# Performance work log

Measured on AMD Instinct MI355X. Metric: run time of the kernel, lower is better.

## Reference

```python
import jax, jax.numpy as jnp
import numpy as np

SHAPES = [(4, 48, 48), (2, 24, 24), (1, 12, 12), (1, 6, 6)]  # (D,H,W) per level
B, E, NH, NL, NP, DF, NLAYERS = 2, 256, 8, 4, 4, 1024, 6
HD = E // NH
LEVEL_SIZES = [d * h * w for d, h, w in SHAPES]
LEVEL_START = [0] + [int(s) for s in np.cumsum(LEVEL_SIZES)[:-1]]
S = int(sum(LEVEL_SIZES))
PARAM_KEYS = ['W_off', 'b_off', 'W_attn', 'b_attn', 'W_val', 'b_val', 'W_out', 'b_out',
              'ln1_g', 'ln1_b', 'W_ff1', 'b_ff1', 'W_ff2', 'b_ff2', 'ln2_g', 'ln2_b']


def setup_inputs() -> dict:
    key = jax.random.key(0)
    ks = jax.random.split(key, 32)
    inp = {}
    for i, (d, h, w) in enumerate(SHAPES):
        inp[f'feat{i}'] = jax.random.normal(ks[i], (B, E, d, h, w), jnp.float32)
        inp[f'pos{i}'] = jax.random.normal(ks[4 + i], (B, E, d, h, w), jnp.float32)
    inp['level_embed'] = jax.random.normal(ks[8], (NL, E), jnp.float32)
    nrm = lambda k, shape, s: jax.random.normal(k, shape, jnp.float32) * s
    inp['W_off'] = nrm(ks[9], (NLAYERS, E, NH * NL * NP * 3), 0.01)
    inp['b_off'] = nrm(ks[10], (NLAYERS, NH * NL * NP * 3), 1.0)
    inp['W_attn'] = nrm(ks[11], (NLAYERS, E, NH * NL * NP), 0.02)
    inp['b_attn'] = jnp.zeros((NLAYERS, NH * NL * NP), jnp.float32)
    inp['W_val'] = nrm(ks[12], (NLAYERS, E, E), E ** -0.5)
    inp['b_val'] = jnp.zeros((NLAYERS, E), jnp.float32)
    inp['W_out'] = nrm(ks[13], (NLAYERS, E, E), E ** -0.5)
    inp['b_out'] = jnp.zeros((NLAYERS, E), jnp.float32)
    inp['ln1_g'] = jnp.ones((NLAYERS, E), jnp.float32)
    inp['ln1_b'] = jnp.zeros((NLAYERS, E), jnp.float32)
    inp['W_ff1'] = nrm(ks[14], (NLAYERS, E, DF), E ** -0.5)
    inp['b_ff1'] = jnp.zeros((NLAYERS, DF), jnp.float32)
    inp['W_ff2'] = nrm(ks[15], (NLAYERS, DF, E), DF ** -0.5)
    inp['b_ff2'] = jnp.zeros((NLAYERS, E), jnp.float32)
    inp['ln2_g'] = jnp.ones((NLAYERS, E), jnp.float32)
    inp['ln2_b'] = jnp.zeros((NLAYERS, E), jnp.float32)
    return inp


def _layer_norm(x, g, b):
    m = jnp.mean(x, -1, keepdims=True)
    v = jnp.mean((x - m) ** 2, -1, keepdims=True)
    return (x - m) * jax.lax.rsqrt(v + 1e-5) * g + b


def _ref_points():
    # all-zero padding masks -> valid_ratios == 1, so reference points are the
    # normalized voxel centers, identical across levels. Returns (S, 3) in (x, y, z).
    refs = []
    for (D, H, W) in SHAPES:
        z = (jnp.arange(D, dtype=jnp.float32) + 0.5) / D
        y = (jnp.arange(H, dtype=jnp.float32) + 0.5) / H
        x = (jnp.arange(W, dtype=jnp.float32) + 0.5) / W
        zz, yy, xx = jnp.meshgrid(z, y, x, indexing='ij')
        refs.append(jnp.stack([xx.ravel(), yy.ravel(), zz.ravel()], -1))
    return jnp.concatenate(refs, 0)


def _sample_level(v, coords, w, D, H, W):
    # v: (B, NH, N_lvl, HD) flattened level values
    # coords: (B, NH, S, NP, 3) pixel-space coords (x, y, z), align_corners=False convention
    # w: (B, NH, S, NP) attention weights (folded into trilinear corner weights)
    cx, cy, cz = coords[..., 0], coords[..., 1], coords[..., 2]
    x0, y0, z0 = jnp.floor(cx), jnp.floor(cy), jnp.floor(cz)
    fx, fy, fz = cx - x0, cy - y0, cz - z0
    Bq, Hq, Sq, Pq = w.shape
    acc = jnp.zeros((Bq, Hq, Sq, HD), v.dtype)
    for dz in (0, 1):
        wz = fz if dz else 1.0 - fz
        iz = z0 + dz
        for dy in (0, 1):
            wy = fy if dy else 1.0 - fy
            iy = y0 + dy
            for dx in (0, 1):
                wx = fx if dx else 1.0 - fx
                ix = x0 + dx
                valid = (ix >= 0) & (ix < W) & (iy >= 0) & (iy < H) & (iz >= 0) & (iz < D)
                wgt = w * wx * wy * wz * valid  # zero-padding outside the volume
                idx = ((jnp.clip(iz, 0, D - 1) * H + jnp.clip(iy, 0, H - 1)) * W
                       + jnp.clip(ix, 0, W - 1)).astype(jnp.int32)
                g = jnp.take_along_axis(v, idx.reshape(Bq, Hq, Sq * Pq)[..., None], axis=2)
                g = g.reshape(Bq, Hq, Sq, Pq, HD)
                acc = acc + jnp.einsum('bhsp,bhspd->bhsd', wgt, g)
    return acc


def _deform_attn(x, pos, ref, normalizer, p, sample_fn):
    B_, S_, _ = x.shape
    q = x + pos
    value = (x @ p['W_val'] + p['b_val']).reshape(B_, S_, NH, HD).transpose(0, 2, 1, 3)
    off = (q @ p['W_off'] + p['b_off']).reshape(B_, S_, NH, NL, NP, 3)
    attn = jax.nn.softmax((q @ p['W_attn'] + p['b_attn']).reshape(B_, S_, NH, NL * NP), -1)
    attn = attn.reshape(B_, S_, NH, NL, NP)
    # normalized sampling locations in [0,1]^3 (x, y, z)
    loc = ref[None, :, None, None, None, :] + off / normalizer[None, None, None, :, None, :]
    out = jnp.zeros((B_, NH, S_, HD), x.dtype)
    for lvl, (D, H, W) in enumerate(SHAPES):
        s0, n = LEVEL_START[lvl], LEVEL_SIZES[lvl]
        v = value[:, :, s0:s0 + n]
        size = jnp.array([W, H, D], x.dtype)
        coords = (loc[:, :, :, lvl] * size - 0.5).transpose(0, 2, 1, 3, 4)  # (B,NH,S,NP,3)
        w = attn[:, :, :, lvl].transpose(0, 2, 1, 3)  # (B,NH,S,NP)
        out = out + sample_fn(v, coords, w, D, H, W)
    out = out.transpose(0, 2, 1, 3).reshape(B_, S_, E)
    return out @ p['W_out'] + p['b_out']


def _encoder_layer(x, pos, ref, normalizer, p, sample_fn):
    x = _layer_norm(x + _deform_attn(x, pos, ref, normalizer, p, sample_fn),
                    p['ln1_g'], p['ln1_b'])
    h = jax.nn.relu(x @ p['W_ff1'] + p['b_ff1']) @ p['W_ff2'] + p['b_ff2']
    return _layer_norm(x + h, p['ln2_g'], p['ln2_b'])


def _forward(feats, poss, level_embed, params, sample_fn):
    x = jnp.concatenate([f.reshape(f.shape[0], E, -1).transpose(0, 2, 1) for f in feats], axis=1)
    pos = jnp.concatenate(
        [poss[l].reshape(poss[l].shape[0], E, -1).transpose(0, 2, 1) + level_embed[l]
         for l in range(NL)], axis=1)
    ref = _ref_points()
    normalizer = jnp.array([[w, h, d] for d, h, w in SHAPES], jnp.float32)  # (NL,3) (x,y,z)
    for l in range(NLAYERS):
        p = {k: params[k][l] for k in PARAM_KEYS}
        x = _encoder_layer(x, pos, ref, normalizer, p, sample_fn)
    return x


def reference(feat0, feat1, feat2, feat3, pos0, pos1, pos2, pos3, level_embed,
              W_off, b_off, W_attn, b_attn, W_val, b_val, W_out, b_out,
              ln1_g, ln1_b, W_ff1, b_ff1, W_ff2, b_ff2, ln2_g, ln2_b):
    params = dict(W_off=W_off, b_off=b_off, W_attn=W_attn, b_attn=b_attn,
                  W_val=W_val, b_val=b_val, W_out=W_out, b_out=b_out,
                  ln1_g=ln1_g, ln1_b=ln1_b, W_ff1=W_ff1, b_ff1=b_ff1,
                  W_ff2=W_ff2, b_ff2=b_ff2, ln2_g=ln2_g, ln2_b=ln2_b)
    return _forward([feat0, feat1, feat2, feat3], [pos0, pos1, pos2, pos3],
                    level_embed, params, _sample_level)
```

## Files before the change

### kernel.cpp

```cpp
#include <hip/hip_runtime.h>

#define S_TOT   10548
#define M_ROWS  21096
#define M_PAD   21120
#define E_DIM   256
#define NH_DIM  8
#define HD_DIM  32
#define DF_DIM  1024
#define NLAYERS 6

typedef unsigned short ushort_t;
typedef __attribute__((ext_vector_type(8))) short bf16x8;
typedef __attribute__((ext_vector_type(4))) float f32x4;

__device__ inline ushort_t f2bf(float f) {
    unsigned u = __float_as_uint(f);
    u += 0x7FFF + ((u >> 16) & 1);
    return (ushort_t)(u >> 16);
}
__device__ inline float bf2f(ushort_t h) {
    return __uint_as_float(((unsigned)h) << 16);
}
__device__ inline f32x4 up2(unsigned a, unsigned b) {
    f32x4 v;
// ... 129 lines not shown
        __syncthreads();
        if (k0 + 32 < K) {
            const int nxt = cur ^ 1;
            gload16(Ag + k0 + 32, (ushort_t*)&As[nxt][(w * 16) * 32]);
            #pragma unroll
            for (int q = 0; q < 4; ++q)
                gload16(Bg + (size_t)(q * 16) * K + k0 + 32,
                        (ushort_t*)&Bs[nxt][(w * 64 + q * 16) * 32]);
        }
        bf16x8 af[4], bfr[4];
        #pragma unroll
        for (int i = 0; i < 4; ++i)
            af[i] = *(const bf16x8*)&As[cur][(i * 16 + lrow) * 32 + rs];
        #pragma unroll
        for (int j = 0; j < 4; ++j)
            bfr[j] = *(const bf16x8*)&Bs[cur][(wn + j * 16 + lrow) * 32 + rs];
        #pragma unroll
        for (int i = 0; i < 4; ++i)
            #pragma unroll
            for (int j = 0; j < 4; ++j)
                acc[i][j] = __builtin_amdgcn_mfma_f32_16x16x32_bf16(af[i], bfr[j], acc[i][j], 0, 0, 0);
    }

    #pragma unroll
    for (int j = 0; j < 4; ++j) {
        int col = wn + j * 16 + lrow;
        float bia = (sup == 0) ? b1[col]
                  : (sup == 1) ? b2[col]
                  : (col < 128) ? b2[256 + col] : b3[col - 128];
        #pragma unroll
        for (int i = 0; i < 4; ++i)
            #pragma unroll
            for (int rg = 0; rg < 4; ++rg) {
                int row = row0 + i * 16 + quad * 4 + rg;
                if (row < M) {
                    float v = acc[i][j][rg] + bia;
                    if (sup == 0) {
                        int b = (row >= S_TOT) ? 1 : 0;
                        int s = row - b * S_TOT;
                        O1[(((size_t)(b * NH_DIM + (col >> 5))) * S_TOT + s) * HD_DIM + (col & 31)] = f2bf(v);
                    } else if (sup == 2 && col >= 128) {
                        int acol = col - 128;
                        O3[((size_t)(acol >> 4) * M_ROWS + row) * 16 + (acol & 15)] = f2bf(v);
                    } else {
                        int ocol = (sup == 1) ? col : 256 + col;
                        int hh = (ocol * 1366) >> 16;
                        O2[((size_t)hh * M_ROWS + row) * 48 + (ocol - hh * 48)] = f2bf(v);
                    }
                }
            }
    }
}

__global__ __launch_bounds__(256, 4)
void gemm_ln(const ushort_t* __restrict__ A, const ushort_t* __restrict__ Bt,
             const float* __restrict__ bias,
             float* __restrict__ x, ushort_t* __restrict__ xb,
             const float* __restrict__ lng, const float* __restrict__ lnb,
             int M)
{
    __shared__ short As[2][32 * 32];
    __shared__ short Bs[2][256 * 32];
    float* red1 = (float*)&As[0][0];
    float* red2 = red1 + 32 * 5;
    const int K = 256;
    int t    = threadIdx.x;
    int row0 = blockIdx.x * 32;
    int lane = t & 63;
    int w    = t >> 6;
    int wn   = w * 64;
    const int quad = lane >> 4, lrow = lane & 15;

    f32x4 acc[2][4];
    #pragma unroll
    for (int i = 0; i < 2; ++i)
        #pragma unroll
        for (int j = 0; j < 4; ++j)
            acc[i][j] = (f32x4){0.f, 0.f, 0.f, 0.f};

    int srow = lane >> 2;
    const int sw = (((lane & 3) ^ ((lane >> 3) & 3)) * 8);
    const int rs = ((quad ^ ((lrow >> 1) & 3)) * 8);
    const ushort_t* Ag = A + (size_t)(row0 + w * 16 + srow) * K + sw;
    const ushort_t* Bg = Bt + (size_t)(w * 64 + srow) * K + sw;

    if (w < 2) gload16(Ag, (ushort_t*)&As[0][(w * 16) * 32]);
    #pragma unroll
    for (int q = 0; q < 4; ++q)
        gload16(Bg + (size_t)(q * 16) * K,
                (ushort_t*)&Bs[0][(w * 64 + q * 16) * 32]);

    #pragma unroll
    for (int k0 = 0; k0 < K; k0 += 32) {
        const int cur = (k0 >> 5) & 1;
        __syncthreads();
        if (k0 + 32 < K) {
            const int nxt = cur ^ 1;
            if (w < 2) gload16(Ag + k0 + 32, (ushort_t*)&As[nxt][(w * 16) * 32]);
            #pragma unroll
            for (int q = 0; q < 4; ++q)
                gload16(Bg + (size_t)(q * 16) * K + k0 + 32,
                        (ushort_t*)&Bs[nxt][(w * 64 + q * 16) * 32]);
        }
        bf16x8 af[2], bfr[4];
        #pragma unroll
        for (int i = 0; i < 2; ++i)
            af[i] = *(const bf16x8*)&As[cur][(i * 16 + lrow) * 32 + rs];
        #pragma unroll
        for (int j = 0; j < 4; ++j)
            bfr[j] = *(const bf16x8*)&Bs[cur][(wn + j * 16 + lrow) * 32 + rs];
        #pragma unroll
        for (int i = 0; i < 2; ++i)
            #pragma unroll
            for (int j = 0; j < 4; ++j)
                acc[i][j] = __builtin_amdgcn_mfma_f32_16x16x32_bf16(af[i], bfr[j], acc[i][j], 0, 0, 0);
    }

    float gj[4], bj[4], bi[4];
    #pragma unroll
    for (int j = 0; j < 4; ++j) {
        int col = wn + j * 16 + lrow;
        gj[j] = lng[col];
        bj[j] = lnb[col];
        bi[j] = bias[col];
    }

    #pragma unroll
    for (int i = 0; i < 2; ++i)
        #pragma unroll
        for (int rg = 0; rg < 4; ++rg) {
            int row = row0 + i * 16 + quad * 4 + rg;
            #pragma unroll
            for (int j = 0; j < 4; ++j) {
                int col = wn + j * 16 + lrow;
                float xres = (row < M) ? x[(size_t)row * 256 + col] : 0.f;
                acc[i][j][rg] += bi[j] + xres;
            }
            float p1 = acc[i][0][rg] + acc[i][1][rg] + acc[i][2][rg] + acc[i][3][rg];
            float p2 = acc[i][0][rg] * acc[i][0][rg] + acc[i][1][rg] * acc[i][1][rg]
                     + acc[i][2][rg] * acc[i][2][rg] + acc[i][3][rg] * acc[i][3][rg];
            p1 += __shfl_xor(p1, 1); p2 += __shfl_xor(p2, 1);
            p1 += __shfl_xor(p1, 2); p2 += __shfl_xor(p2, 2);
            p1 += __shfl_xor(p1, 4); p2 += __shfl_xor(p2, 4);
            p1 += __shfl_xor(p1, 8); p2 += __shfl_xor(p2, 8);
            if (lrow == 0) {
                int rl = i * 16 + quad * 4 + rg;
                red1[rl * 5 + w] = p1;
                red2[rl * 5 + w] = p2;
            }
        }
    __syncthreads();

    #pragma unroll
    for (int i = 0; i < 2; ++i)
        #pragma unroll
        for (int rg = 0; rg < 4; ++rg) {
            int rl = i * 16 + quad * 4 + rg;
            float S1 = red1[rl * 5 + 0] + red1[rl * 5 + 1] + red1[rl * 5 + 2] + red1[rl * 5 + 3];
            float S2 = red2[rl * 5 + 0] + red2[rl * 5 + 1] + red2[rl * 5 + 2] + red2[rl * 5 + 3];
            float mean = S1 * (1.f / 256);
            float rstd = rsqrtf(S2 * (1.f / 256) - mean * mean + 1e-5f);
            int row = row0 + rl;
            if (row < M) {
                #pragma unroll
                for (int j = 0; j < 4; ++j) {
                    int col = wn + j * 16 + lrow;
                    float out = (acc[i][j][rg] - mean) * rstd * gj[j] + bj[j];
                    size_t o = (size_t)row * 256 + col;
                    x[o]  = out;
                    xb[o] = f2bf(out);
                }
            }
        }
}

__global__ __launch_bounds__(256, 2)
void ffn_kernel(const ushort_t* __restrict__ Axb, const ushort_t* __restrict__ W1t,
                const ushort_t* __restrict__ W2t,
                const float* __restrict__ bias1, const float* __restrict__ bias2,
                float* __restrict__ x, ushort_t* __restrict__ xb,
                ushort_t* __restrict__ qb, const ushort_t* __restrict__ posb,
                const float* __restrict__ lng, const float* __restrict__ lnb,
                int M)
{
    __shared__ short As[2][32 * 32];
    __shared__ short Bs[2][256 * 32];
    __shared__ short Hs[32 * 264];
    float* red1 = (float*)&As[0][0];
    float* red2 = red1 + 32 * 5;
    const int K = 256;
    int t    = threadIdx.x;
    int row0 = blockIdx.x * 32;
    int lane = t & 63;
    int w    = t >> 6;
    int wn   = w * 64;
    const int quad = lane >> 4, lrow = lane & 15;
    int srow = lane >> 2;
    const int sw = (((lane & 3) ^ ((lane >> 3) & 3)) * 8);
    const int rs = ((quad ^ ((lrow >> 1) & 3)) * 8);

    f32x4 acc[2][4];
    #pragma unroll
    for (int i = 0; i < 2; ++i)
        #pragma unroll
        for (int j = 0; j < 4; ++j)
            acc[i][j] = (f32x4){0.f, 0.f, 0.f, 0.f};

    const ushort_t* Ag = Axb + (size_t)(row0 + w * 16 + srow) * K + sw;

    for (int c = 0; c < 4; ++c) {
        f32x4 hh[2][4];
        #pragma unroll
        for (int i = 0; i < 2; ++i)
            #pragma unroll
            for (int j = 0; j < 4; ++j)
                hh[i][j] = (f32x4){0.f, 0.f, 0.f, 0.f};

        const ushort_t* B1g = W1t + (size_t)(c * 256 + w * 64 + srow) * K + sw;

        __syncthreads();
        if (w < 2) gload16(Ag, (ushort_t*)&As[0][(w * 16) * 32]);
        #pragma unroll
        for (int q = 0; q < 4; ++q)
            gload16(B1g + (size_t)(q * 16) * K,
                    (ushort_t*)&Bs[0][(w * 64 + q * 16) * 32]);

        #pragma unroll
        for (int k0 = 0; k0 < K; k0 += 32) {
            const int cur = (k0 >> 5) & 1;
            __syncthreads();
            if (k0 + 32 < K) {
                const int nxt = cur ^ 1;
                if (w < 2) gload16(Ag + k0 + 32, (ushort_t*)&As[nxt][(w * 16) * 32]);
                #pragma unroll
                for (int q = 0; q < 4; ++q)
                    gload16(B1g + (size_t)(q * 16) * K + k0 + 32,
                            (ushort_t*)&Bs[nxt][(w * 64 + q * 16) * 32]);
            }
            bf16x8 af[2], bfr[4];
            #pragma unroll
            for (int i = 0; i < 2; ++i)
                af[i] = *(const bf16x8*)&As[cur][(i * 16 + lrow) * 32 + rs];
            #pragma unroll
            for (int j = 0; j < 4; ++j)
                bfr[j] = *(const bf16x8*)&Bs[cur][(wn + j * 16 + lrow) * 32 + rs];
            #pragma unroll
            for (int i = 0; i < 2; ++i)
                #pragma unroll
                for (int j = 0; j < 4; ++j)
                    hh[i][j] = __builtin_amdgcn_mfma_f32_16x16x32_bf16(af[i], bfr[j], hh[i][j], 0, 0, 0);
        }

        #pragma unroll
        for (int j = 0; j < 4; ++j) {
            int col = wn + j * 16 + lrow;
            float b1v = bias1[c * 256 + col];
            #pragma unroll
            for (int i = 0; i < 2; ++i)
                #pragma unroll
                for (int rg = 0; rg < 4; ++rg) {
                    int rl = i * 16 + quad * 4 + rg;
                    Hs[rl * 264 + col] = f2bf(fmaxf(hh[i][j][rg] + b1v, 0.f));
                }
        }
        __syncthreads();

        const ushort_t* B2g = W2t + (size_t)(w * 64 + srow) * 1024 + c * 256 + sw;
        #pragma unroll
        for (int q = 0; q < 4; ++q)
            gload16(B2g + (size_t)(q * 16) * 1024,
                    (ushort_t*)&Bs[0][(w * 64 + q * 16) * 32]);

        #pragma unroll
        for (int k0 = 0; k0 < 256; k0 += 32) {
            const int cur = (k0 >> 5) & 1;
            __syncthreads();
            if (k0 + 32 < 256) {
                const int nxt = cur ^ 1;
                #pragma unroll
                for (int q = 0; q < 4; ++q)
                    gload16(B2g + (size_t)(q * 16) * 1024 + k0 + 32,
                            (ushort_t*)&Bs[nxt][(w * 64 + q * 16) * 32]);
            }
            bf16x8 af[2], bfr[4];
            #pragma unroll
            for (int i = 0; i < 2; ++i)
                af[i] = *(const bf16x8*)&Hs[(i * 16 + lrow) * 264 + k0 + quad * 8];
            #pragma unroll
            for (int j = 0; j < 4; ++j)
                bfr[j] = *(const bf16x8*)&Bs[cur][(wn + j * 16 + lrow) * 32 + rs];
            #pragma unroll
            for (int i = 0; i < 2; ++i)
                #pragma unroll
                for (int j = 0; j < 4; ++j)
                    acc[i][j] = __builtin_amdgcn_mfma_f32_16x16x32_bf16(af[i], bfr[j], acc[i][j], 0, 0, 0);
        }
    }

    float gj[4], bj[4], bi[4];
    #pragma unroll
    for (int j = 0; j < 4; ++j) {
        int col = wn + j * 16 + lrow;
        gj[j] = lng[col];
        bj[j] = lnb[col];
        bi[j] = bias2[col];
    }

    #pragma unroll
    for (int i = 0; i < 2; ++i)
        #pragma unroll
        for (int rg = 0; rg < 4; ++rg) {
            int row = row0 + i * 16 + quad * 4 + rg;
            #pragma unroll
            for (int j = 0; j < 4; ++j) {
                int col = wn + j * 16 + lrow;
                float xres = (row < M) ? x[(size_t)row * 256 + col] : 0.f;
                acc[i][j][rg] += bi[j] + xres;
            }
            float p1 = acc[i][0][rg] + acc[i][1][rg] + acc[i][2][rg] + acc[i][3][rg];
            float p2 = acc[i][0][rg] * acc[i][0][rg] + acc[i][1][rg] * acc[i][1][rg]
                     + acc[i][2][rg] * acc[i][2][rg] + acc[i][3][rg] * acc[i][3][rg];
            p1 += __shfl_xor(p1, 1); p2 += __shfl_xor(p2, 1);
            p1 += __shfl_xor(p1, 2); p2 += __shfl_xor(p2, 2);
            p1 += __shfl_xor(p1, 4); p2 += __shfl_xor(p2, 4);
            p1 += __shfl_xor(p1, 8); p2 += __shfl_xor(p2, 8);
            if (lrow == 0) {
                int rl = i * 16 + quad * 4 + rg;
                red1[rl * 5 + w] = p1;
                red2[rl * 5 + w] = p2;
            }
        }
    __syncthreads();

    #pragma unroll
    for (int i = 0; i < 2; ++i)
        #pragma unroll
        for (int rg = 0; rg < 4; ++rg) {
            int rl = i * 16 + quad * 4 + rg;
            float S1 = red1[rl * 5 + 0] + red1[rl * 5 + 1] + red1[rl * 5 + 2] + red1[rl * 5 + 3];
            float S2 = red2[rl * 5 + 0] + red2[rl * 5 + 1] + red2[rl * 5 + 2] + red2[rl * 5 + 3];
            float mean = S1 * (1.f / 256);
            float rstd = rsqrtf(S2 * (1.f / 256) - mean * mean + 1e-5f);
            int row = row0 + rl;
            if (row < M) {
                #pragma unroll
                for (int j = 0; j < 4; ++j) {
                    int col = wn + j * 16 + lrow;
                    float out = (acc[i][j][rg] - mean) * rstd * gj[j] + bj[j];
                    size_t o = (size_t)row * 256 + col;
                    x[o]  = out;
                    xb[o] = f2bf(out);
                    qb[o] = f2bf(out + bf2f(posb[o]));
                }
            }
        }
}

__global__ __launch_bounds__(256, 4)
void sample_kernel(const ushort_t* __restrict__ valueb,
                   const ushort_t* __restrict__ offh,
                   const ushort_t* __restrict__ attnh,
                   ushort_t* __restrict__ sampb)
{
    __shared__ float wrec[16 * 168];
    __shared__ int   idxA[16 * 40];

    const int LD_[4]  = {4, 2, 1, 1};
    const int LH_[4]  = {48, 24, 12, 6};
    const int LW_[4]  = {48, 24, 12, 6};
    const int LS0_[4] = {0, 9216, 10368, 10512};

    int t   = threadIdx.x;
    int gl  = t >> 4;
    int sub = t & 15;
    int h   = blockIdx.x;
    int r   = blockIdx.y * 16 + gl;
    bool valid = (r < M_ROWS);
    if (!valid) r = M_ROWS - 1;
    int b   = (r >= S_TOT) ? 1 : 0;
    int s   = r - b * S_TOT;

    float rx, ry, rz;
    {
        int j;
        if (s < 9216)       { j = s;         int qx = j % 48; int q2 = j / 48; int qy = q2 % 48; int qz = q2 / 48;
                              rx = (qx + 0.5f) * (1.f/48); ry = (qy + 0.5f) * (1.f/48); rz = (qz + 0.5f) * (1.f/4); }
        else if (s < 10368) { j = s - 9216;  int qx = j % 24; int q2 = j / 24; int qy = q2 % 24; int qz = q2 / 24;
                              rx = (qx + 0.5f) * (1.f/24); ry = (qy + 0.5f) * (1.f/24); rz = (qz + 0.5f) * (1.f/2); }
        else if (s < 10512) { j = s - 10368; int qx = j % 12; int qy = j / 12;
                              rx = (qx + 0.5f) * (1.f/12); ry = (qy + 0.5f) * (1.f/12); rz = 0.5f; }
        else                { j = s - 10512; int qx = j % 6;  int qy = j / 6;
                              rx = (qx + 0.5f) * (1.f/6);  ry = (qy + 0.5f) * (1.f/6);  rz = 0.5f; }
    }

    {
        int p = sub;
        float lg = bf2f(attnh[((size_t)h * M_ROWS + r) * 16 + p]);
        float mx = lg;
        mx = fmaxf(mx, __shfl_xor(mx, 1));
        mx = fmaxf(mx, __shfl_xor(mx, 2));
        mx = fmaxf(mx, __shfl_xor(mx, 4));
        mx = fmaxf(mx, __shfl_xor(mx, 8));
        float e = __expf(lg - mx);
        float sm = e;
        sm += __shfl_xor(sm, 1);
        sm += __shfl_xor(sm, 2);
        sm += __shfl_xor(sm, 4);
        sm += __shfl_xor(sm, 8);
// ... 60 lines not shown
    accA.z += __shfl_xor(accA.z, 8); accA.w += __shfl_xor(accA.w, 8);
    accB.x += __shfl_xor(accB.x, 8); accB.y += __shfl_xor(accB.y, 8);
    accB.z += __shfl_xor(accB.z, 8); accB.w += __shfl_xor(accB.w, 8);

    if (cr == 0 && valid) {
        ushort4 o1, o2;
        o1.x = f2bf(accA.x); o1.y = f2bf(accA.y); o1.z = f2bf(accA.z); o1.w = f2bf(accA.w);
        o2.x = f2bf(accB.x); o2.y = f2bf(accB.y); o2.z = f2bf(accB.z); o2.w = f2bf(accB.w);
        ushort_t* op = sampb + (size_t)r * E_DIM + h * HD_DIM + q * 8;
        *(ushort4*)op       = o1;
        *(ushort4*)(op + 4) = o2;
    }
}

extern "C" void kernel_launch(void* const* d_in, const int* in_sizes, int n_in,
                              void* d_out, int out_size, void* d_ws, size_t ws_size,
                              hipStream_t stream)
{
    const float* f0     = (const float*)d_in[0];
    const float* p0     = (const float*)d_in[1];
    const float* f1     = (const float*)d_in[2];
    const float* p1     = (const float*)d_in[3];
    const float* f2     = (const float*)d_in[4];
    const float* p2     = (const float*)d_in[5];
    const float* f3     = (const float*)d_in[6];
    const float* p3     = (const float*)d_in[7];
    const float* lemb   = (const float*)d_in[8];
    const float* W_off  = (const float*)d_in[9];
    const float* b_off  = (const float*)d_in[10];
    const float* W_attn = (const float*)d_in[11];
    const float* b_attn = (const float*)d_in[12];
    const float* W_val  = (const float*)d_in[13];
    const float* b_val  = (const float*)d_in[14];
    const float* W_out  = (const float*)d_in[15];
    const float* b_out  = (const float*)d_in[16];
    const float* ln1_g  = (const float*)d_in[17];
    const float* ln1_b  = (const float*)d_in[18];
    const float* W_ff1  = (const float*)d_in[19];
    const float* b_ff1  = (const float*)d_in[20];
    const float* W_ff2  = (const float*)d_in[21];
    const float* b_ff2  = (const float*)d_in[22];
    const float* ln2_g  = (const float*)d_in[23];
    const float* ln2_b  = (const float*)d_in[24];

    float* x = (float*)d_out;
    char*  w = (char*)d_ws;

    ushort_t* posb   = (ushort_t*)(w + 0);
    ushort_t* valueb = (ushort_t*)(w + 21626880 + 262144);
    char*     region =            (w + 34525184);
    ushort_t* offh   = (ushort_t*)(region);
    ushort_t* attnh  = (ushort_t*)(region + 16220160);
    ushort_t* sampb  = (ushort_t*)(region + 21626880);
    ushort_t* xb     = (ushort_t*)(w + 77778944);
    ushort_t* qb     = (ushort_t*)(w + 88592384);
    ushort_t* wb     = (ushort_t*)(w + 99405824);

    ushort_t* Wc_t = wb;
    ushort_t* Wp_t = wb + 1179648;
    ushort_t* W1_t = wb + 1572864;
    ushort_t* W2_t = wb + 3145728;

    dim3 blk(256);

    transpose_cvt_kernel<<<dim3(8, 8, 6),  blk, 0, stream>>>(W_val,  Wc_t, 256, 256,  196608, 0);
    transpose_cvt_kernel<<<dim3(12, 8, 6), blk, 0, stream>>>(W_off,  Wc_t, 256, 384,  196608, 256);
    transpose_cvt_kernel<<<dim3(4, 8, 6),  blk, 0, stream>>>(W_attn, Wc_t, 256, 128,  196608, 640);
    transpose_cvt_kernel<<<dim3(8, 8, 6),  blk, 0, stream>>>(W_out,  Wp_t, 256, 256,   65536, 0);
    transpose_cvt_kernel<<<dim3(32, 8, 6), blk, 0, stream>>>(W_ff1,  W1_t, 256, 1024, 262144, 0);
    transpose_cvt_kernel<<<dim3(8, 32, 6), blk, 0, stream>>>(W_ff2,  W2_t, 1024, 256, 262144, 0);

    assemble_kernel<<<dim3(331, 8, 2), blk, 0, stream>>>(
        f0, p0, f1, p1, f2, p2, f3, p3, lemb, x, posb, xb, qb);

    const int MT = M_PAD / 64;
    const int LT = M_PAD / 32;
    const int SB = (M_ROWS + 15) / 16;
    for (int l = 0; l < NLAYERS; ++l) {
        gemm_part1<<<dim3(3, MT), blk, 0, stream>>>(
            xb, qb, Wc_t + l * 196608,
            b_val + l * 256, b_off + l * 384, b_attn + l * 128,
            valueb, offh, attnh, M_ROWS);
        sample_kernel<<<dim3(NH_DIM, SB), blk, 0, stream>>>(valueb, offh, attnh, sampb);
        gemm_ln<<<LT, blk, 0, stream>>>(
            sampb, Wp_t + l * 65536, b_out + l * 256,
            x, xb, ln1_g + l * 256, ln1_b + l * 256, M_ROWS);
        ffn_kernel<<<LT, blk, 0, stream>>>(
            xb, W1_t + l * 262144, W2_t + l * 262144,
            b_ff1 + l * 1024, b_ff2 + l * 256,
            x, xb, qb, posb,
            ln2_g + l * 256, ln2_b + l * 256, M_ROWS);
    }
}
```

Before: 1.116 ms.

## Fuse output projection and LayerNorm1 into the FFN kernel

Merges the output-projection GEMM with its residual add and first LayerNorm into the FFN kernel. The normalized rows stay in a shared-memory tile (Xs) that feeds the FFN's first GEMM, and the fp32 residual stays in registers for the second LayerNorm. This removes one kernel launch per layer and the global write and re-read of x/xb between the two stages. In exchange the fused kernel needs more registers and shared memory, which may reduce occupancy.

```diff
diff --git a/kernel.cpp b/kernel.cpp
--- a/kernel.cpp
+++ b/kernel.cpp
@@ -205,140 +205,21 @@
     }
 }
 
-__global__ __launch_bounds__(256, 4)
-void gemm_ln(const ushort_t* __restrict__ A, const ushort_t* __restrict__ Bt,
-             const float* __restrict__ bias,
-             float* __restrict__ x, ushort_t* __restrict__ xb,
-             const float* __restrict__ lng, const float* __restrict__ lnb,
-             int M)
-{
-    __shared__ short As[2][32 * 32];
-    __shared__ short Bs[2][256 * 32];
-    float* red1 = (float*)&As[0][0];
-    float* red2 = red1 + 32 * 5;
-    const int K = 256;
-    int t    = threadIdx.x;
-    int row0 = blockIdx.x * 32;
-    int lane = t & 63;
-    int w    = t >> 6;
-    int wn   = w * 64;
-    const int quad = lane >> 4, lrow = lane & 15;
-
-    f32x4 acc[2][4];
-    #pragma unroll
-    for (int i = 0; i < 2; ++i)
-        #pragma unroll
-        for (int j = 0; j < 4; ++j)
-            acc[i][j] = (f32x4){0.f, 0.f, 0.f, 0.f};
-
-    int srow = lane >> 2;
-    const int sw = (((lane & 3) ^ ((lane >> 3) & 3)) * 8);
-    const int rs = ((quad ^ ((lrow >> 1) & 3)) * 8);
-    const ushort_t* Ag = A + (size_t)(row0 + w * 16 + srow) * K + sw;
-    const ushort_t* Bg = Bt + (size_t)(w * 64 + srow) * K + sw;
-
-    if (w < 2) gload16(Ag, (ushort_t*)&As[0][(w * 16) * 32]);
-    #pragma unroll
-    for (int q = 0; q < 4; ++q)
-        gload16(Bg + (size_t)(q * 16) * K,
-                (ushort_t*)&Bs[0][(w * 64 + q * 16) * 32]);
-
-    #pragma unroll
-    for (int k0 = 0; k0 < K; k0 += 32) {
-        const int cur = (k0 >> 5) & 1;
-        __syncthreads();
-        if (k0 + 32 < K) {
-            const int nxt = cur ^ 1;
-            if (w < 2) gload16(Ag + k0 + 32, (ushort_t*)&As[nxt][(w * 16) * 32]);
-            #pragma unroll
-            for (int q = 0; q < 4; ++q)
-                gload16(Bg + (size_t)(q * 16) * K + k0 + 32,
-                        (ushort_t*)&Bs[nxt][(w * 64 + q * 16) * 32]);
-        }
-        bf16x8 af[2], bfr[4];
-        #pragma unroll
-        for (int i = 0; i < 2; ++i)
-            af[i] = *(const bf16x8*)&As[cur][(i * 16 + lrow) * 32 + rs];
-        #pragma unroll
-        for (int j = 0; j < 4; ++j)
-            bfr[j] = *(const bf16x8*)&Bs[cur][(wn + j * 16 + lrow) * 32 + rs];
-        #pragma unroll
-        for (int i = 0; i < 2; ++i)
-            #pragma unroll
-            for (int j = 0; j < 4; ++j)
-                acc[i][j] = __builtin_amdgcn_mfma_f32_16x16x32_bf16(af[i], bfr[j], acc[i][j], 0, 0, 0);
-    }
-
-    float gj[4], bj[4], bi[4];
-    #pragma unroll
-    for (int j = 0; j < 4; ++j) {
-        int col = wn + j * 16 + lrow;
-        gj[j] = lng[col];
-        bj[j] = lnb[col];
-        bi[j] = bias[col];
-    }
-
-    #pragma unroll
-    for (int i = 0; i < 2; ++i)
-        #pragma unroll
-        for (int rg = 0; rg < 4; ++rg) {
-            int row = row0 + i * 16 + quad * 4 + rg;
-            #pragma unroll
-            for (int j = 0; j < 4; ++j) {
-                int col = wn + j * 16 + lrow;
-                float xres = (row < M) ? x[(size_t)row * 256 + col] : 0.f;
-                acc[i][j][rg] += bi[j] + xres;
-            }
-            float p1 = acc[i][0][rg] + acc[i][1][rg] + acc[i][2][rg] + acc[i][3][rg];
-            float p2 = acc[i][0][rg] * acc[i][0][rg] + acc[i][1][rg] * acc[i][1][rg]
-                     + acc[i][2][rg] * acc[i][2][rg] + acc[i][3][rg] * acc[i][3][rg];
-            p1 += __shfl_xor(p1, 1); p2 += __shfl_xor(p2, 1);
-            p1 += __shfl_xor(p1, 2); p2 += __shfl_xor(p2, 2);
-            p1 += __shfl_xor(p1, 4); p2 += __shfl_xor(p2, 4);
-            p1 += __shfl_xor(p1, 8); p2 += __shfl_xor(p2, 8);
-            if (lrow == 0) {
-                int rl = i * 16 + quad * 4 + rg;
-                red1[rl * 5 + w] = p1;
-                red2[rl * 5 + w] = p2;
-            }
-        }
-    __syncthreads();
-
-    #pragma unroll
-    for (int i = 0; i < 2; ++i)
-        #pragma unroll
-        for (int rg = 0; rg < 4; ++rg) {
-            int rl = i * 16 + quad * 4 + rg;
-            float S1 = red1[rl * 5 + 0] + red1[rl * 5 + 1] + red1[rl * 5 + 2] + red1[rl * 5 + 3];
-            float S2 = red2[rl * 5 + 0] + red2[rl * 5 + 1] + red2[rl * 5 + 2] + red2[rl * 5 + 3];
-            float mean = S1 * (1.f / 256);
-            float rstd = rsqrtf(S2 * (1.f / 256) - mean * mean + 1e-5f);
-            int row = row0 + rl;
-            if (row < M) {
-                #pragma unroll
-                for (int j = 0; j < 4; ++j) {
-                    int col = wn + j * 16 + lrow;
-                    float out = (acc[i][j][rg] - mean) * rstd * gj[j] + bj[j];
-                    size_t o = (size_t)row * 256 + col;
-                    x[o]  = out;
-                    xb[o] = f2bf(out);
-                }
-            }
-        }
-}
-
 __global__ __launch_bounds__(256, 2)
-void ffn_kernel(const ushort_t* __restrict__ Axb, const ushort_t* __restrict__ W1t,
-                const ushort_t* __restrict__ W2t,
-                const float* __restrict__ bias1, const float* __restrict__ bias2,
-                float* __restrict__ x, ushort_t* __restrict__ xb,
-                ushort_t* __restrict__ qb, const ushort_t* __restrict__ posb,
-                const float* __restrict__ lng, const float* __restrict__ lnb,
-                int M)
+void ln_ffn_kernel(const ushort_t* __restrict__ Asamp, const ushort_t* __restrict__ Wpt,
+                   const float* __restrict__ biasP,
+                   const float* __restrict__ ln1g, const float* __restrict__ ln1b,
+                   const ushort_t* __restrict__ W1t, const ushort_t* __restrict__ W2t,
+                   const float* __restrict__ bias1, const float* __restrict__ bias2,
+                   float* __restrict__ x, ushort_t* __restrict__ xb,
+                   ushort_t* __restrict__ qb, const ushort_t* __restrict__ posb,
+                   const float* __restrict__ ln2g, const float* __restrict__ ln2b,
+                   int M)
 {
     __shared__ short As[2][32 * 32];
     __shared__ short Bs[2][256 * 32];
     __shared__ short Hs[32 * 264];
+    __shared__ short Xs[32 * 264];
     float* red1 = (float*)&As[0][0];
     float* red2 = red1 + 32 * 5;
     const int K = 256;
@@ -352,30 +233,21 @@
     const int sw = (((lane & 3) ^ ((lane >> 3) & 3)) * 8);
     const int rs = ((quad ^ ((lrow >> 1) & 3)) * 8);
 
-    f32x4 acc[2][4];
+    f32x4 accL[2][4];
     #pragma unroll
     for (int i = 0; i < 2; ++i)
         #pragma unroll
         for (int j = 0; j < 4; ++j)
-            acc[i][j] = (f32x4){0.f, 0.f, 0.f, 0.f};
-
-    const ushort_t* Ag = Axb + (size_t)(row0 + w * 16 + srow) * K + sw;
-
-    for (int c = 0; c < 4; ++c) {
-        f32x4 hh[2][4];
-        #pragma unroll
-        for (int i = 0; i < 2; ++i)
-            #pragma unroll
-            for (int j = 0; j < 4; ++j)
-                hh[i][j] = (f32x4){0.f, 0.f, 0.f, 0.f};
-
-        const ushort_t* B1g = W1t + (size_t)(c * 256 + w * 64 + srow) * K + sw;
-
-        __syncthreads();
+            accL[i][j] = (f32x4){0.f, 0.f, 0.f, 0.f};
+
+    {
+        const ushort_t* Ag = Asamp + (size_t)(row0 + w * 16 + srow) * K + sw;
+        const ushort_t* Bg = Wpt + (size_t)(w * 64 + srow) * K + sw;
+
         if (w < 2) gload16(Ag, (ushort_t*)&As[0][(w * 16) * 32]);
         #pragma unroll
         for (int q = 0; q < 4; ++q)
-            gload16(B1g + (size_t)(q * 16) * K,
+            gload16(Bg + (size_t)(q * 16) * K,
                     (ushort_t*)&Bs[0][(w * 64 + q * 16) * 32]);
 
         #pragma unroll
@@ -387,13 +259,118 @@
                 if (w < 2) gload16(Ag + k0 + 32, (ushort_t*)&As[nxt][(w * 16) * 32]);
                 #pragma unroll
                 for (int q = 0; q < 4; ++q)
+                    gload16(Bg + (size_t)(q * 16) * K + k0 + 32,
+                            (ushort_t*)&Bs[nxt][(w * 64 + q * 16) * 32]);
+            }
+            bf16x8 af[2], bfr[4];
+            #pragma unroll
+            for (int i = 0; i < 2; ++i)
+                af[i] = *(const bf16x8*)&As[cur][(i * 16 + lrow) * 32 + rs];
+            #pragma unroll
+            for (int j = 0; j < 4; ++j)
+                bfr[j] = *(const bf16x8*)&Bs[cur][(wn + j * 16 + lrow) * 32 + rs];
+            #pragma unroll
+            for (int i = 0; i < 2; ++i)
+                #pragma unroll
+                for (int j = 0; j < 4; ++j)
+                    accL[i][j] = __builtin_amdgcn_mfma_f32_16x16x32_bf16(af[i], bfr[j], accL[i][j], 0, 0, 0);
+        }
+    }
+
+    f32x4 resid[2][4];
+    {
+        float gj[4], bj[4], bi[4];
+        #pragma unroll
+        for (int j = 0; j < 4; ++j) {
+            int col = wn + j * 16 + lrow;
+            gj[j] = ln1g[col];
+            bj[j] = ln1b[col];
+            bi[j] = biasP[col];
+        }
+
+        #pragma unroll
+        for (int i = 0; i < 2; ++i)
+            #pragma unroll
+            for (int rg = 0; rg < 4; ++rg) {
+                int row = row0 + i * 16 + quad * 4 + rg;
+                #pragma unroll
+                for (int j = 0; j < 4; ++j) {
+                    int col = wn + j * 16 + lrow;
+                    float xres = (row < M) ? x[(size_t)row * 256 + col] : 0.f;
+                    accL[i][j][rg] += bi[j] + xres;
+                }
+                float p1 = accL[i][0][rg] + accL[i][1][rg] + accL[i][2][rg] + accL[i][3][rg];
+                float p2 = accL[i][0][rg] * accL[i][0][rg] + accL[i][1][rg] * accL[i][1][rg]
+                         + accL[i][2][rg] * accL[i][2][rg] + accL[i][3][rg] * accL[i][3][rg];
+                p1 += __shfl_xor(p1, 1); p2 += __shfl_xor(p2, 1);
+                p1 += __shfl_xor(p1, 2); p2 += __shfl_xor(p2, 2);
+                p1 += __shfl_xor(p1, 4); p2 += __shfl_xor(p2, 4);
+                p1 += __shfl_xor(p1, 8); p2 += __shfl_xor(p2, 8);
+                if (lrow == 0) {
+                    int rl = i * 16 + quad * 4 + rg;
+                    red1[rl * 5 + w] = p1;
+                    red2[rl * 5 + w] = p2;
+                }
+            }
+        __syncthreads();
+
+        #pragma unroll
+        for (int i = 0; i < 2; ++i)
+            #pragma unroll
+            for (int rg = 0; rg < 4; ++rg) {
+                int rl = i * 16 + quad * 4 + rg;
+                float S1 = red1[rl * 5 + 0] + red1[rl * 5 + 1] + red1[rl * 5 + 2] + red1[rl * 5 + 3];
+                float S2 = red2[rl * 5 + 0] + red2[rl * 5 + 1] + red2[rl * 5 + 2] + red2[rl * 5 + 3];
+                float mean = S1 * (1.f / 256);
+                float rstd = rsqrtf(S2 * (1.f / 256) - mean * mean + 1e-5f);
+                #pragma unroll
+                for (int j = 0; j < 4; ++j) {
+                    int col = wn + j * 16 + lrow;
+                    float out = (accL[i][j][rg] - mean) * rstd * gj[j] + bj[j];
+                    resid[i][j][rg] = out;
+                    Xs[rl * 264 + col] = f2bf(out);
+                }
+            }
+    }
+
+    f32x4 acc[2][4];
+    #pragma unroll
+    for (int i = 0; i < 2; ++i)
+        #pragma unroll
+        for (int j = 0; j < 4; ++j)
+            acc[i][j] = (f32x4){0.f, 0.f, 0.f, 0.f};
+
+    for (int c = 0; c < 4; ++c) {
+        f32x4 hh[2][4];
+        #pragma unroll
+        for (int i = 0; i < 2; ++i)
+            #pragma unroll
+            for (int j = 0; j < 4; ++j)
+                hh[i][j] = (f32x4){0.f, 0.f, 0.f, 0.f};
+
+        const ushort_t* B1g = W1t + (size_t)(c * 256 + w * 64 + srow) * K + sw;
+
+        __syncthreads();
+        #pragma unroll
+        for (int q = 0; q < 4; ++q)
+            gload16(B1g + (size_t)(q * 16) * K,
+                    (ushort_t*)&Bs[0][(w * 64 + q * 16) * 32]);
+
+        #pragma unroll
+        for (int k0 = 0; k0 < K; k0 += 32) {
+            const int cur = (k0 >> 5) & 1;
+            __syncthreads();
+            if (k0 + 32 < K) {
+                const int nxt = cur ^ 1;
+                #pragma unroll
+                for (int q = 0; q < 4; ++q)
                     gload16(B1g + (size_t)(q * 16) * K + k0 + 32,
                             (ushort_t*)&Bs[nxt][(w * 64 + q * 16) * 32]);
             }
             bf16x8 af[2], bfr[4];
             #pragma unroll
             for (int i = 0; i < 2; ++i)
-                af[i] = *(const bf16x8*)&As[cur][(i * 16 + lrow) * 32 + rs];
+                af[i] = *(const bf16x8*)&Xs[(i * 16 + lrow) * 264 + k0 + quad * 8];
             #pragma unroll
             for (int j = 0; j < 4; ++j)
                 bfr[j] = *(const bf16x8*)&Bs[cur][(wn + j * 16 + lrow) * 32 + rs];
@@ -450,63 +427,61 @@
         }
     }
 
-    float gj[4], bj[4], bi[4];
-    #pragma unroll
-    for (int j = 0; j < 4; ++j) {
-        int col = wn + j * 16 + lrow;
-        gj[j] = lng[col];
-        bj[j] = lnb[col];
-        bi[j] = bias2[col];
-    }
-
-    #pragma unroll
-    for (int i = 0; i < 2; ++i)
-        #pragma unroll
-        for (int rg = 0; rg < 4; ++rg) {
-            int row = row0 + i * 16 + quad * 4 + rg;
-            #pragma unroll
-            for (int j = 0; j < 4; ++j) {
-                int col = wn + j * 16 + lrow;
-                float xres = (row < M) ? x[(size_t)row * 256 + col] : 0.f;
-                acc[i][j][rg] += bi[j] + xres;
-            }
-            float p1 = acc[i][0][rg] + acc[i][1][rg] + acc[i][2][rg] + acc[i][3][rg];
-            float p2 = acc[i][0][rg] * acc[i][0][rg] + acc[i][1][rg] * acc[i][1][rg]
-                     + acc[i][2][rg] * acc[i][2][rg] + acc[i][3][rg] * acc[i][3][rg];
-            p1 += __shfl_xor(p1, 1); p2 += __shfl_xor(p2, 1);
-            p1 += __shfl_xor(p1, 2); p2 += __shfl_xor(p2, 2);
-            p1 += __shfl_xor(p1, 4); p2 += __shfl_xor(p2, 4);
-            p1 += __shfl_xor(p1, 8); p2 += __shfl_xor(p2, 8);
-            if (lrow == 0) {
+    {
+        float gj[4], bj[4], bi[4];
+        #pragma unroll
+        for (int j = 0; j < 4; ++j) {
+            int col = wn + j * 16 + lrow;
+            gj[j] = ln2g[col];
+            bj[j] = ln2b[col];
+            bi[j] = bias2[col];
+        }
+
+        #pragma unroll
+        for (int i = 0; i < 2; ++i)
+            #pragma unroll
+            for (int rg = 0; rg < 4; ++rg) {
+                #pragma unroll
+                for (int j = 0; j < 4; ++j)
+                    acc[i][j][rg] += bi[j] + resid[i][j][rg];
+                float p1 = acc[i][0][rg] + acc[i][1][rg] + acc[i][2][rg] + acc[i][3][rg];
+                float p2 = acc[i][0][rg] * acc[i][0][rg] + acc[i][1][rg] * acc[i][1][rg]
+                         + acc[i][2][rg] * acc[i][2][rg] + acc[i][3][rg] * acc[i][3][rg];
+                p1 += __shfl_xor(p1, 1); p2 += __shfl_xor(p2, 1);
+                p1 += __shfl_xor(p1, 2); p2 += __shfl_xor(p2, 2);
+                p1 += __shfl_xor(p1, 4); p2 += __shfl_xor(p2, 4);
+                p1 += __shfl_xor(p1, 8); p2 += __shfl_xor(p2, 8);
+                if (lrow == 0) {
+                    int rl = i * 16 + quad * 4 + rg;
+                    red1[rl * 5 + w] = p1;
+                    red2[rl * 5 + w] = p2;
+                }
+            }
+        __syncthreads();
+
+        #pragma unroll
+        for (int i = 0; i < 2; ++i)
+            #pragma unroll
+            for (int rg = 0; rg < 4; ++rg) {
                 int rl = i * 16 + quad * 4 + rg;
-                red1[rl * 5 + w] = p1;
-                red2[rl * 5 + w] = p2;
-            }
-        }
-    __syncthreads();
-
-    #pragma unroll
-    for (int i = 0; i < 2; ++i)
-        #pragma unroll
-        for (int rg = 0; rg < 4; ++rg) {
-            int rl = i * 16 + quad * 4 + rg;
-            float S1 = red1[rl * 5 + 0] + red1[rl * 5 + 1] + red1[rl * 5 + 2] + red1[rl * 5 + 3];
-            float S2 = red2[rl * 5 + 0] + red2[rl * 5 + 1] + red2[rl * 5 + 2] + red2[rl * 5 + 3];
-            float mean = S1 * (1.f / 256);
-            float rstd = rsqrtf(S2 * (1.f / 256) - mean * mean + 1e-5f);
-            int row = row0 + rl;
-            if (row < M) {
-                #pragma unroll
-                for (int j = 0; j < 4; ++j) {
-                    int col = wn + j * 16 + lrow;
-                    float out = (acc[i][j][rg] - mean) * rstd * gj[j] + bj[j];
-                    size_t o = (size_t)row * 256 + col;
-                    x[o]  = out;
-                    xb[o] = f2bf(out);
-                    qb[o] = f2bf(out + bf2f(posb[o]));
+                float S1 = red1[rl * 5 + 0] + red1[rl * 5 + 1] + red1[rl * 5 + 2] + red1[rl * 5 + 3];
+                float S2 = red2[rl * 5 + 0] + red2[rl * 5 + 1] + red2[rl * 5 + 2] + red2[rl * 5 + 3];
+                float mean = S1 * (1.f / 256);
+                float rstd = rsqrtf(S2 * (1.f / 256) - mean * mean + 1e-5f);
+                int row = row0 + rl;
+                if (row < M) {
+                    #pragma unroll
+                    for (int j = 0; j < 4; ++j) {
+                        int col = wn + j * 16 + lrow;
+                        float out = (acc[i][j][rg] - mean) * rstd * gj[j] + bj[j];
+                        size_t o = (size_t)row * 256 + col;
+                        x[o]  = out;
+                        xb[o] = f2bf(out);
+                        qb[o] = f2bf(out + bf2f(posb[o]));
+                    }
                 }
             }
-        }
+    }
 }
 
 __global__ __launch_bounds__(256, 4)
@@ -703,11 +678,10 @@
             b_val + l * 256, b_off + l * 384, b_attn + l * 128,
             valueb, offh, attnh, M_ROWS);
         sample_kernel<<<dim3(NH_DIM, SB), blk, 0, stream>>>(valueb, offh, attnh, sampb);
-        gemm_ln<<<LT, blk, 0, stream>>>(
+        ln_ffn_kernel<<<LT, blk, 0, stream>>>(
             sampb, Wp_t + l * 65536, b_out + l * 256,
-            x, xb, ln1_g + l * 256, ln1_b + l * 256, M_ROWS);
-        ffn_kernel<<<LT, blk, 0, stream>>>(
-            xb, W1_t + l * 262144, W2_t + l * 262144,
+            ln1_g + l * 256, ln1_b + l * 256,
+            W1_t + l * 262144, W2_t + l * 262144,
             b_ff1 + l * 1024, b_ff2 + l * 256,
             x, xb, qb, posb,
             ln2_g + l * 256, ln2_b + l * 256, M_ROWS);
```

After: 1.242 ms. +11.4%, slower.

## Split fused FFN into two GEMM kernels with a global bf16 hidden buffer

Applied to the files above, without the earlier changes.

Replaces the fused FFN kernel, which kept the 32x1024 hidden activation in shared memory in four chunks, with two kernels. The first computes relu(xW1+b1) into a global bf16 hidden buffer that reuses the offset/attention scratch region. The second runs a K=1024 GEMM plus bias, residual and LayerNorm. Both use 64-row tiles with 4 blocks per CU, giving more weight reuse per tile and more parallelism in the first GEMM. The cost is writing and re-reading a roughly 43MB hidden tensor through global memory and one extra launch per layer.

```diff
diff --git a/kernel.cpp b/kernel.cpp
--- a/kernel.cpp
+++ b/kernel.cpp
@@ -327,127 +327,147 @@
         }
 }
 
-__global__ __launch_bounds__(256, 2)
-void ffn_kernel(const ushort_t* __restrict__ Axb, const ushort_t* __restrict__ W1t,
-                const ushort_t* __restrict__ W2t,
-                const float* __restrict__ bias1, const float* __restrict__ bias2,
-                float* __restrict__ x, ushort_t* __restrict__ xb,
-                ushort_t* __restrict__ qb, const ushort_t* __restrict__ posb,
-                const float* __restrict__ lng, const float* __restrict__ lnb,
-                int M)
+__global__ __launch_bounds__(256, 4)
+void ffn1_kernel(const ushort_t* __restrict__ A, const ushort_t* __restrict__ W1t,
+                 const float* __restrict__ bias1, ushort_t* __restrict__ hid,
+                 int M)
 {
-    __shared__ short As[2][32 * 32];
+    __shared__ short As[2][64 * 32];
     __shared__ short Bs[2][256 * 32];
-    __shared__ short Hs[32 * 264];
-    float* red1 = (float*)&As[0][0];
-    float* red2 = red1 + 32 * 5;
     const int K = 256;
     int t    = threadIdx.x;
-    int row0 = blockIdx.x * 32;
+    int nc   = blockIdx.x;
+    int row0 = blockIdx.y * 64;
     int lane = t & 63;
     int w    = t >> 6;
     int wn   = w * 64;
     const int quad = lane >> 4, lrow = lane & 15;
+
+    f32x4 acc[4][4];
+    #pragma unroll
+    for (int i = 0; i < 4; ++i)
+        #pragma unroll
+        for (int j = 0; j < 4; ++j)
+            acc[i][j] = (f32x4){0.f, 0.f, 0.f, 0.f};
+
     int srow = lane >> 2;
     const int sw = (((lane & 3) ^ ((lane >> 3) & 3)) * 8);
     const int rs = ((quad ^ ((lrow >> 1) & 3)) * 8);
-
-    f32x4 acc[2][4];
-    #pragma unroll
-    for (int i = 0; i < 2; ++i)
+    const ushort_t* Ag = A + (size_t)(row0 + w * 16 + srow) * K + sw;
+    const ushort_t* Bg = W1t + (size_t)(nc * 256 + w * 64 + srow) * K + sw;
+
+    gload16(Ag, (ushort_t*)&As[0][(w * 16) * 32]);
+    #pragma unroll
+    for (int q = 0; q < 4; ++q)
+        gload16(Bg + (size_t)(q * 16) * K,
+                (ushort_t*)&Bs[0][(w * 64 + q * 16) * 32]);
+
+    #pragma unroll
+    for (int k0 = 0; k0 < K; k0 += 32) {
+        const int cur = (k0 >> 5) & 1;
+        __syncthreads();
+        if (k0 + 32 < K) {
+            const int nxt = cur ^ 1;
+            gload16(Ag + k0 + 32, (ushort_t*)&As[nxt][(w * 16) * 32]);
+            #pragma unroll
+            for (int q = 0; q < 4; ++q)
+                gload16(Bg + (size_t)(q * 16) * K + k0 + 32,
+                        (ushort_t*)&Bs[nxt][(w * 64 + q * 16) * 32]);
+        }
+        bf16x8 af[4], bfr[4];
+        #pragma unroll
+        for (int i = 0; i < 4; ++i)
+            af[i] = *(const bf16x8*)&As[cur][(i * 16 + lrow) * 32 + rs];
+        #pragma unroll
+        for (int j = 0; j < 4; ++j)
+            bfr[j] = *(const bf16x8*)&Bs[cur][(wn + j * 16 + lrow) * 32 + rs];
+        #pragma unroll
+        for (int i = 0; i < 4; ++i)
+            #pragma unroll
+            for (int j = 0; j < 4; ++j)
+                acc[i][j] = __builtin_amdgcn_mfma_f32_16x16x32_bf16(af[i], bfr[j], acc[i][j], 0, 0, 0);
+    }
+
+    #pragma unroll
+    for (int j = 0; j < 4; ++j) {
+        int col  = wn + j * 16 + lrow;
+        int gcol = nc * 256 + col;
+        float b1v = bias1[gcol];
+        #pragma unroll
+        for (int i = 0; i < 4; ++i)
+            #pragma unroll
+            for (int rg = 0; rg < 4; ++rg) {
+                int row = row0 + i * 16 + quad * 4 + rg;
+                if (row < M)
+                    hid[(size_t)row * 1024 + gcol] =
+                        f2bf(fmaxf(acc[i][j][rg] + b1v, 0.f));
+            }
+    }
+}
+
+__global__ __launch_bounds__(256, 4)
+void ffn2_kernel(const ushort_t* __restrict__ hid, const ushort_t* __restrict__ W2t,
+                 const float* __restrict__ bias2,
+                 float* __restrict__ x, ushort_t* __restrict__ xb,
+                 ushort_t* __restrict__ qb, const ushort_t* __restrict__ posb,
+                 const float* __restrict__ lng, const float* __restrict__ lnb,
+                 int M)
+{
+    __shared__ short As[2][64 * 32];
+    __shared__ short Bs[2][256 * 32];
+    float* red1 = (float*)&As[0][0];
+    float* red2 = red1 + 64 * 5;
+    const int K = 1024;
+    int t    = threadIdx.x;
+    int row0 = blockIdx.x * 64;
+    int lane = t & 63;
+    int w    = t >> 6;
+    int wn   = w * 64;
+    const int quad = lane >> 4, lrow = lane & 15;
+
+    f32x4 acc[4][4];
+    #pragma unroll
+    for (int i = 0; i < 4; ++i)
         #pragma unroll
         for (int j = 0; j < 4; ++j)
             acc[i][j] = (f32x4){0.f, 0.f, 0.f, 0.f};
 
-    const ushort_t* Ag = Axb + (size_t)(row0 + w * 16 + srow) * K + sw;
-
-    for (int c = 0; c < 4; ++c) {
-        f32x4 hh[2][4];
-        #pragma unroll
-        for (int i = 0; i < 2; ++i)
+    int srow = lane >> 2;
+    const int sw = (((lane & 3) ^ ((lane >> 3) & 3)) * 8);
+    const int rs = ((quad ^ ((lrow >> 1) & 3)) * 8);
+    const ushort_t* Ag = hid + (size_t)(row0 + w * 16 + srow) * K + sw;
+    const ushort_t* Bg = W2t + (size_t)(w * 64 + srow) * K + sw;
+
+    gload16(Ag, (ushort_t*)&As[0][(w * 16) * 32]);
+    #pragma unroll
+    for (int q = 0; q < 4; ++q)
+        gload16(Bg + (size_t)(q * 16) * K,
+                (ushort_t*)&Bs[0][(w * 64 + q * 16) * 32]);
+
+    #pragma unroll 4
+    for (int k0 = 0; k0 < K; k0 += 32) {
+        const int cur = (k0 >> 5) & 1;
+        __syncthreads();
+        if (k0 + 32 < K) {
+            const int nxt = cur ^ 1;
+            gload16(Ag + k0 + 32, (ushort_t*)&As[nxt][(w * 16) * 32]);
+            #pragma unroll
+            for (int q = 0; q < 4; ++q)
+                gload16(Bg + (size_t)(q * 16) * K + k0 + 32,
+                        (ushort_t*)&Bs[nxt][(w * 64 + q * 16) * 32]);
+        }
+        bf16x8 af[4], bfr[4];
+        #pragma unroll
+        for (int i = 0; i < 4; ++i)
+            af[i] = *(const bf16x8*)&As[cur][(i * 16 + lrow) * 32 + rs];
+        #pragma unroll
+        for (int j = 0; j < 4; ++j)
+            bfr[j] = *(const bf16x8*)&Bs[cur][(wn + j * 16 + lrow) * 32 + rs];
+        #pragma unroll
+        for (int i = 0; i < 4; ++i)
             #pragma unroll
             for (int j = 0; j < 4; ++j)
-                hh[i][j] = (f32x4){0.f, 0.f, 0.f, 0.f};
-
-        const ushort_t* B1g = W1t + (size_t)(c * 256 + w * 64 + srow) * K + sw;
-
-        __syncthreads();
-        if (w < 2) gload16(Ag, (ushort_t*)&As[0][(w * 16) * 32]);
-        #pragma unroll
-        for (int q = 0; q < 4; ++q)
-            gload16(B1g + (size_t)(q * 16) * K,
-                    (ushort_t*)&Bs[0][(w * 64 + q * 16) * 32]);
-
-        #pragma unroll
-        for (int k0 = 0; k0 < K; k0 += 32) {
-            const int cur = (k0 >> 5) & 1;
-            __syncthreads();
-            if (k0 + 32 < K) {
-                const int nxt = cur ^ 1;
-                if (w < 2) gload16(Ag + k0 + 32, (ushort_t*)&As[nxt][(w * 16) * 32]);
-                #pragma unroll
-                for (int q = 0; q < 4; ++q)
-                    gload16(B1g + (size_t)(q * 16) * K + k0 + 32,
-                            (ushort_t*)&Bs[nxt][(w * 64 + q * 16) * 32]);
-            }
-            bf16x8 af[2], bfr[4];
-            #pragma unroll
-            for (int i = 0; i < 2; ++i)
-                af[i] = *(const bf16x8*)&As[cur][(i * 16 + lrow) * 32 + rs];
-            #pragma unroll
-            for (int j = 0; j < 4; ++j)
-                bfr[j] = *(const bf16x8*)&Bs[cur][(wn + j * 16 + lrow) * 32 + rs];
-            #pragma unroll
-            for (int i = 0; i < 2; ++i)
-                #pragma unroll
-                for (int j = 0; j < 4; ++j)
-                    hh[i][j] = __builtin_amdgcn_mfma_f32_16x16x32_bf16(af[i], bfr[j], hh[i][j], 0, 0, 0);
-        }
-
-        #pragma unroll
-        for (int j = 0; j < 4; ++j) {
-            int col = wn + j * 16 + lrow;
-            float b1v = bias1[c * 256 + col];
-            #pragma unroll
-            for (int i = 0; i < 2; ++i)
-                #pragma unroll
-                for (int rg = 0; rg < 4; ++rg) {
-                    int rl = i * 16 + quad * 4 + rg;
-                    Hs[rl * 264 + col] = f2bf(fmaxf(hh[i][j][rg] + b1v, 0.f));
-                }
-        }
-        __syncthreads();
-
-        const ushort_t* B2g = W2t + (size_t)(w * 64 + srow) * 1024 + c * 256 + sw;
-        #pragma unroll
-        for (int q = 0; q < 4; ++q)
-            gload16(B2g + (size_t)(q * 16) * 1024,
-                    (ushort_t*)&Bs[0][(w * 64 + q * 16) * 32]);
-
-        #pragma unroll
-        for (int k0 = 0; k0 < 256; k0 += 32) {
-            const int cur = (k0 >> 5) & 1;
-            __syncthreads();
-            if (k0 + 32 < 256) {
-                const int nxt = cur ^ 1;
-                #pragma unroll
-                for (int q = 0; q < 4; ++q)
-                    gload16(B2g + (size_t)(q * 16) * 1024 + k0 + 32,
-                            (ushort_t*)&Bs[nxt][(w * 64 + q * 16) * 32]);
-            }
-            bf16x8 af[2], bfr[4];
-            #pragma unroll
-            for (int i = 0; i < 2; ++i)
-                af[i] = *(const bf16x8*)&Hs[(i * 16 + lrow) * 264 + k0 + quad * 8];
-            #pragma unroll
-            for (int j = 0; j < 4; ++j)
-                bfr[j] = *(const bf16x8*)&Bs[cur][(wn + j * 16 + lrow) * 32 + rs];
-            #pragma unroll
-            for (int i = 0; i < 2; ++i)
-                #pragma unroll
-                for (int j = 0; j < 4; ++j)
-                    acc[i][j] = __builtin_amdgcn_mfma_f32_16x16x32_bf16(af[i], bfr[j], acc[i][j], 0, 0, 0);
-        }
+                acc[i][j] = __builtin_amdgcn_mfma_f32_16x16x32_bf16(af[i], bfr[j], acc[i][j], 0, 0, 0);
     }
 
     float gj[4], bj[4], bi[4];
@@ -460,7 +480,7 @@
     }
 
     #pragma unroll
-    for (int i = 0; i < 2; ++i)
+    for (int i = 0; i < 4; ++i)
         #pragma unroll
         for (int rg = 0; rg < 4; ++rg) {
             int row = row0 + i * 16 + quad * 4 + rg;
@@ -486,7 +506,7 @@
     __syncthreads();
 
     #pragma unroll
-    for (int i = 0; i < 2; ++i)
+    for (int i = 0; i < 4; ++i)
         #pragma unroll
         for (int rg = 0; rg < 4; ++rg) {
             int rl = i * 16 + quad * 4 + rg;
@@ -673,6 +693,7 @@
     ushort_t* offh   = (ushort_t*)(region);
     ushort_t* attnh  = (ushort_t*)(region + 16220160);
     ushort_t* sampb  = (ushort_t*)(region + 21626880);
+    ushort_t* hidden = (ushort_t*)(region);
     ushort_t* xb     = (ushort_t*)(w + 77778944);
     ushort_t* qb     = (ushort_t*)(w + 88592384);
     ushort_t* wb     = (ushort_t*)(w + 99405824);
@@ -706,9 +727,10 @@
         gemm_ln<<<LT, blk, 0, stream>>>(
             sampb, Wp_t + l * 65536, b_out + l * 256,
             x, xb, ln1_g + l * 256, ln1_b + l * 256, M_ROWS);
-        ffn_kernel<<<LT, blk, 0, stream>>>(
-            xb, W1_t + l * 262144, W2_t + l * 262144,
-            b_ff1 + l * 1024, b_ff2 + l * 256,
+        ffn1_kernel<<<dim3(4, MT), blk, 0, stream>>>(
+            xb, W1_t + l * 262144, b_ff1 + l * 1024, hidden, M_ROWS);
+        ffn2_kernel<<<MT, blk, 0, stream>>>(
+            hidden, W2_t + l * 262144, b_ff2 + l * 256,
             x, xb, qb, posb,
             ln2_g + l * 256, ln2_b + l * 256, M_ROWS);
     }
```

Measured after the change: 1.297 ms. +16.2%, slower.
